# Performance work log

Measured on AMD Instinct MI355X. Metric: run time of the kernel, lower is better.

Reference implementation:

```python
import jax, jax.numpy as jnp
import numpy as np
import math

NUM_HEADS = 16
ROPE_BASE = 10000.0
SLIDING_WINDOW = 512  # note: original triu-then-tril composition makes the mask empty (no-op)


def _rope_cos_sin(seq_len, head_dim, dtype):
    inv_freq = 1.0 / (ROPE_BASE ** (jnp.arange(0, head_dim, 2, dtype=jnp.float32) / head_dim))
    t = jnp.arange(seq_len, dtype=jnp.float32)
    freqs = t[:, None] * inv_freq[None, :]          # [S, D/2]
    emb = jnp.concatenate([freqs, freqs], axis=-1)  # [S, D]
    # reshape to broadcast over [B, S, H, D]
    return jnp.cos(emb)[None, :, None, :].astype(dtype), jnp.sin(emb)[None, :, None, :].astype(dtype)


def _rotate_half(x):
    x1, x2 = jnp.split(x, 2, axis=-1)
    return jnp.concatenate([-x2, x1], axis=-1)


def setup_inputs() -> dict:
    key = jax.random.key(0)
    ks = jax.random.split(key, 9)
    B, S, E = 2, 2048, 2048
    sc = 1.0 / math.sqrt(E)
    return {
        "hidden_states": jax.random.normal(ks[0], (B, S, E), dtype=jnp.float32),
        "Wq": jax.random.normal(ks[1], (E, E), dtype=jnp.float32) * sc,
        "bq": jax.random.normal(ks[2], (E,), dtype=jnp.float32) * 0.01,
        "Wk": jax.random.normal(ks[3], (E, E), dtype=jnp.float32) * sc,
        "bk": jax.random.normal(ks[4], (E,), dtype=jnp.float32) * 0.01,
        "Wv": jax.random.normal(ks[5], (E, E), dtype=jnp.float32) * sc,
        "bv": jax.random.normal(ks[6], (E,), dtype=jnp.float32) * 0.01,
        "Wo": jax.random.normal(ks[7], (E, E), dtype=jnp.float32) * sc,
        "bo": jax.random.normal(ks[8], (E,), dtype=jnp.float32) * 0.01,
    }


def reference(hidden_states, Wq, bq, Wk, bk, Wv, bv, Wo, bo):
    B, S, E = hidden_states.shape
    H = NUM_HEADS
    D = E // H
    q = (hidden_states @ Wq.T + bq).reshape(B, S, H, D)
    k = (hidden_states @ Wk.T + bk).reshape(B, S, H, D)
    v = (hidden_states @ Wv.T + bv).reshape(B, S, H, D)

    cos, sin = _rope_cos_sin(S, D, q.dtype)
    q = q * cos + _rotate_half(q) * sin
    k = k * cos + _rotate_half(k) * sin

    scale = 1.0 / math.sqrt(D)
    scores = jnp.einsum("bqhd,bkhd->bhqk", q, k) * scale  # [B,H,S,S]
    # Faithful to source: triu(ones, +w) followed by tril(..., -w) is empty -> mask is a no-op.
    attn = jax.nn.softmax(scores, axis=-1)
    out = jnp.einsum("bhqk,bkhd->bqhd", attn, v).reshape(B, S, E)
    return out @ Wo.T + bo
```

## Files before the change

kernel.cpp:

```cpp
#include <hip/hip_runtime.h>
#include <hip/hip_bf16.h>

#define B_ 2
#define S_ 2048
#define E_ 2048
#define H_ 16
#define D_ 128
#define M_ (B_*S_)
#define NQKV_ (3*E_)

typedef __attribute__((ext_vector_type(8))) short bf16x8;
typedef __attribute__((ext_vector_type(4))) float f32x4;
typedef __attribute__((ext_vector_type(4))) unsigned short u16x4;
typedef __attribute__((ext_vector_type(2))) unsigned u32x2;

__device__ __forceinline__ unsigned short f2bf(float f) {
  union { float f; unsigned u; } v; v.f = f;
  unsigned r = v.u + 0x7fffu + ((v.u >> 16) & 1u);
  return (unsigned short)(r >> 16);
}
__device__ __forceinline__ float bf2f(unsigned short h) {
  union { unsigned u; float f; } v; v.u = ((unsigned)h) << 16;
  return v.f;
}

__device__ __forceinline__ void gload_lds16(const void* g, void* l) {
  __builtin_amdgcn_global_load_lds(
      (const __attribute__((address_space(1))) unsigned*)g,
      (__attribute__((address_space(3))) unsigned*)l, 16, 0, 0);
}

__global__ __launch_bounds__(256) void prep_kernel(
    const float* __restrict__ hs,
    const float* __restrict__ Wq, const float* __restrict__ Wk, const float* __restrict__ Wv,
    const float* __restrict__ Wo,
    const float* __restrict__ bq, const float* __restrict__ bk, const float* __restrict__ bv,
    unsigned short* __restrict__ hsb, unsigned short* __restrict__ Wqkv,
    unsigned short* __restrict__ Wob, float* __restrict__ biasqkv,
    float* __restrict__ cosT, float* __restrict__ sinT)
{
  const int seg = blockIdx.y;
  const int t0 = blockIdx.x * 256 + threadIdx.x;
  const int stride = gridDim.x * 256;
  if (seg == 0) {
    const int n = (M_*E_)/4;
    for (int i = t0; i < n; i += stride) {
      f32x4 v = ((const f32x4*)hs)[i];
      u16x4 o; o[0]=f2bf(v[0]); o[1]=f2bf(v[1]); o[2]=f2bf(v[2]); o[3]=f2bf(v[3]);
      ((u16x4*)hsb)[i] = o;
    }
  } else if (seg == 1) {
    const int n = (3*E_*E_)/4;
    for (int i = t0; i < n; i += stride) {
      int e4 = i << 2;
      int r = e4 >> 11;
      int k = e4 & 2047;
      const float* src = (r < E_) ? (Wq + ((size_t)r << 11) + k)
                       : (r < 2*E_) ? (Wk + ((size_t)(r - E_) << 11) + k)
                       : (Wv + ((size_t)(r - 2*E_) << 11) + k);
      f32x4 v = *(const f32x4*)src;
      u16x4 o; o[0]=f2bf(v[0]); o[1]=f2bf(v[1]); o[2]=f2bf(v[2]); o[3]=f2bf(v[3]);
      ((u16x4*)Wqkv)[i] = o;
    }
  } else if (seg == 2) {
    const int n = (E_*E_)/4;
    for (int i = t0; i < n; i += stride) {
      f32x4 v = ((const f32x4*)Wo)[i];
      u16x4 o; o[0]=f2bf(v[0]); o[1]=f2bf(v[1]); o[2]=f2bf(v[2]); o[3]=f2bf(v[3]);
      ((u16x4*)Wob)[i] = o;
    }
  } else if (seg == 3) {
    for (int i = t0; i < NQKV_; i += stride)
      biasqkv[i] = (i < E_) ? bq[i] : (i < 2*E_) ? bk[i - E_] : bv[i - 2*E_];
  } else {
    for (int i = t0; i < S_*64; i += stride) {
      int j = i & 63, s = i >> 6;
      float inv = exp2f(-(float)j * (13.287712379549449f / 64.0f));
      float ang = (float)s * inv;
      cosT[i] = cosf(ang);
      sinT[i] = sinf(ang);
    }
  }
}

#define STAGE8(basePtr, BUF, AB, KS, KT) do { \
    unsigned short* dst_ = lds + (BUF)*32768 + (AB)*16384 + (KS)*8192; \
    const unsigned short* src_ = (basePtr) + (KT)*64 + (KS)*32; \
    _Pragma("unroll") \
    for (int j_ = 0; j_ < 2; ++j_) { \
      int cc_ = (j_ << 9) + tid; \
      int row_ = cc_ >> 2, c2_ = cc_ & 3; \
      int sc_ = c2_ ^ ((row_ >> 1) & 3); \
      gload_lds16(src_ + (size_t)row_*K + sc_*8, (char*)dst_ + cc_*16); \
    } } while(0)

#define LOADA8(DST, MH, KS, BUF) do { \
    const unsigned short* Ab_ = lds + (BUF)*32768 + (KS)*8192; \
    _Pragma("unroll") \
    for (int j_ = 0; j_ < 4; ++j_) { \
      int row_ = wr*128 + ((MH)*4 + j_)*16 + l15; \
      DST[j_] = *(const bf16x8*)(Ab_ + row_*32 + ((l4 ^ ((row_>>1)&3)) << 3)); \
    } } while(0)

#define LOADB8(DST, KS, BUF) do { \
    const unsigned short* Bb_ = lds + (BUF)*32768 + 16384 + (KS)*8192; \
    _Pragma("unroll") \
    for (int j_ = 0; j_ < 4; ++j_) { \
      int row_ = wc*64 + j_*16 + l15; \
      DST[j_] = *(const bf16x8*)(Bb_ + row_*32 + ((l4 ^ ((row_>>1)&3)) << 3)); \
    } } while(0)

#define PRIO_MFMA(MH, AF, BF) do { \
    __builtin_amdgcn_s_setprio(1); \
    _Pragma("unroll") \
    for (int mm_ = 0; mm_ < 4; ++mm_) \
      _Pragma("unroll") \
      for (int nn_ = 0; nn_ < 4; ++nn_) \
        acc[(MH)*4+mm_][nn_] = __builtin_amdgcn_mfma_f32_16x16x32_bf16(AF[mm_], BF[nn_], acc[(MH)*4+mm_][nn_], 0,0,0); \
    __builtin_amdgcn_s_setprio(0); \
  } while(0)

#define BARPIN do { \
    __builtin_amdgcn_sched_barrier(0); \
    __builtin_amdgcn_s_barrier(); \
    __builtin_amdgcn_sched_barrier(0); \
  } while(0)

__global__ __launch_bounds__(512, 2) void gemm8(
    const unsigned short* __restrict__ A,
    const unsigned short* __restrict__ Bm,
    const float* __restrict__ bias,
    unsigned short* __restrict__ Cv,
    int M, int N, int K)
{
  __shared__ __align__(16) unsigned short lds[65536];
  const int tid = threadIdx.x;
  const int lane = tid & 63;
  const int w = tid >> 6;
  const int wr = w >> 2, wc = w & 3;
  const int l15 = lane & 15, l4 = lane >> 4;

  const int ntile = N >> 8;
  int wg = blockIdx.x;
  const int cpx = gridDim.x >> 3;
  wg = (wg & 7) * cpx + (wg >> 3);
  const int tm = wg / ntile, tn = wg % ntile;

  const unsigned short* Abase = A + ((size_t)tm*256)*K;
  const unsigned short* Bbase = Bm + ((size_t)tn*256)*K;

  f32x4 acc[8][4] = {};
  bf16x8 afA[4], afB[4], bfA[4], bfB[4];

  const int NITER = K >> 7;

  STAGE8(Bbase, 0, 1, 0, 0); STAGE8(Abase, 0, 0, 0, 0);
  STAGE8(Bbase, 0, 1, 1, 0); STAGE8(Abase, 0, 0, 1, 0);
  STAGE8(Bbase, 1, 1, 0, 1); STAGE8(Abase, 1, 0, 0, 1);
  STAGE8(Bbase, 1, 1, 1, 1);
  __builtin_amdgcn_sched_barrier(0);
  asm volatile("s_waitcnt vmcnt(6)" ::: "memory");
  __builtin_amdgcn_s_barrier();
  __builtin_amdgcn_sched_barrier(0);

  for (int i = 0; i < NITER; ++i) {
    const int t1k = 2*i + 1, t2k = 2*i + 2, t3k = 2*i + 3;
    const bool nl = (i < NITER - 1);
    STAGE8(Abase, 1, 0, 1, t1k);
    LOADA8(afA, 0, 0, 0); LOADB8(bfA, 0, 0);
    LOADA8(afB, 1, 0, 0);
    PRIO_MFMA(0, afA, bfA);
    BARPIN;
    if (nl) STAGE8(Bbase, 0, 1, 0, t2k);
    LOADA8(afA, 0, 1, 0); LOADB8(bfB, 1, 0);
    PRIO_MFMA(1, afB, bfA);
    BARPIN;
    if (nl) STAGE8(Abase, 0, 0, 0, t2k);
    LOADA8(afB, 1, 1, 0);
    PRIO_MFMA(0, afA, bfB);
    BARPIN;
    if (nl) STAGE8(Bbase, 0, 1, 1, t2k);
    PRIO_MFMA(1, afB, bfB);
    __builtin_amdgcn_sched_barrier(0);
    if (nl) asm volatile("s_waitcnt vmcnt(6)" ::: "memory");
    else    asm volatile("s_waitcnt vmcnt(0)" ::: "memory");
    __builtin_amdgcn_s_barrier();
    __builtin_amdgcn_sched_barrier(0);
    if (nl) STAGE8(Abase, 0, 0, 1, t2k);
    LOADA8(afA, 0, 0, 1); LOADB8(bfA, 0, 1);
    LOADA8(afB, 1, 0, 1);
    PRIO_MFMA(0, afA, bfA);
    BARPIN;
    if (nl) STAGE8(Bbase, 1, 1, 0, t3k);
    LOADA8(afA, 0, 1, 1); LOADB8(bfB, 1, 1);
    PRIO_MFMA(1, afB, bfA);
    BARPIN;
    if (nl) STAGE8(Abase, 1, 0, 0, t3k);
    LOADA8(afB, 1, 1, 1);
    PRIO_MFMA(0, afA, bfB);
    BARPIN;
    if (nl) STAGE8(Bbase, 1, 1, 1, t3k);
    PRIO_MFMA(1, afB, bfB);
    __builtin_amdgcn_sched_barrier(0);
    if (nl) asm volatile("s_waitcnt vmcnt(6)" ::: "memory");
    else    asm volatile("s_waitcnt vmcnt(0)" ::: "memory");
    __builtin_amdgcn_s_barrier();
    __builtin_amdgcn_sched_barrier(0);
  }

  #pragma unroll
  for (int mt = 0; mt < 8; ++mt) {
    #pragma unroll
    for (int nt = 0; nt < 4; ++nt) {
      int colg = tn*256 + wc*64 + nt*16 + l15;
      float bvv = bias[colg];
      #pragma unroll
      for (int r = 0; r < 4; ++r) {
        int rowg = tm*256 + wr*128 + mt*16 + l4*4 + r;
        Cv[(size_t)rowg*N + colg] = f2bf(acc[mt][nt][r] + bvv);
      }
    }
  }
}

template<int OUT_F32>
__global__ __launch_bounds__(256) void gemm_bt(
    const unsigned short* __restrict__ A,
    const unsigned short* __restrict__ Bm,
    const float* __restrict__ bias,
    void* __restrict__ Cv,
    int M, int N, int K)
{
  __shared__ unsigned short lA[128*64];
  __shared__ unsigned short lB[128*64];
  const int tid = threadIdx.x;
  const int lane = tid & 63;
  const int w = tid >> 6;
  const int wr = w >> 1, wc = w & 1;
  const int ntile = N >> 7;
  const int tm = blockIdx.x / ntile, tn = blockIdx.x % ntile;
  const int l15 = lane & 15, l4 = lane >> 4;

  f32x4 acc[4][4] = {};

  for (int kt = 0; kt < K; kt += 64) {
    #pragma unroll
    for (int i = 0; i < 4; ++i) {
      int cc = i*256 + tid;
      int row = cc >> 3, col = cc & 7;
      int scol = col ^ (row & 7);
      gload_lds16(A + (size_t)(tm*128 + row)*K + kt + scol*8, (char*)lA + cc*16);
    }
    #pragma unroll
    for (int i = 0; i < 4; ++i) {
      int cc = i*256 + tid;
      int row = cc >> 3, col = cc & 7;
      int scol = col ^ (row & 7);
      gload_lds16(Bm + (size_t)(tn*128 + row)*K + kt + scol*8, (char*)lB + cc*16);
    }
    asm volatile("s_waitcnt vmcnt(0)" ::: "memory");
    __syncthreads();

    #pragma unroll
    for (int ks = 0; ks < 2; ++ks) {
      bf16x8 af[4], bfr[4];
      #pragma unroll
      for (int mt = 0; mt < 4; ++mt) {
        int row = wr*64 + mt*16 + l15;
        int ch = (ks*4 + l4) ^ (row & 7);
        af[mt] = *(const bf16x8*)(lA + row*64 + ch*8);
      }
      #pragma unroll
      for (int nt = 0; nt < 4; ++nt) {
        int row = wc*64 + nt*16 + l15;
        int ch = (ks*4 + l4) ^ (row & 7);
        bfr[nt] = *(const bf16x8*)(lB + row*64 + ch*8);
      }
      #pragma unroll
      for (int mt = 0; mt < 4; ++mt)
        #pragma unroll
        for (int nt = 0; nt < 4; ++nt)
          acc[mt][nt] = __builtin_amdgcn_mfma_f32_16x16x32_bf16(af[mt], bfr[nt], acc[mt][nt], 0, 0, 0);
    }
    __syncthreads();
  }

  #pragma unroll
  for (int mt = 0; mt < 4; ++mt) {
    #pragma unroll
    for (int nt = 0; nt < 4; ++nt) {
      int colg = tn*128 + wc*64 + nt*16 + l15;
      float bvv = bias[colg];
      #pragma unroll
      for (int r = 0; r < 4; ++r) {
        int rowg = tm*128 + wr*64 + mt*16 + l4*4 + r;
        float v = acc[mt][nt][r] + bvv;
        if (OUT_F32) ((float*)Cv)[(size_t)rowg*N + colg] = v;
        else ((unsigned short*)Cv)[(size_t)rowg*N + colg] = f2bf(v);
      }
    }
  }
}

__global__ __launch_bounds__(256) void rope_kernel(
    unsigned short* __restrict__ qkv, const float* __restrict__ cosT, const float* __restrict__ sinT)
{
  int t = blockIdx.x*256 + threadIdx.x;
  int i  = t & 63;
  int h  = (t >> 6) & 15;
  int m  = t >> 10;
  int s  = m & (S_-1);
  float c = cosT[s*64 + i], sn = sinT[s*64 + i];
  const float scale = 0.08838834764831845f * 1.4426950408889634f;
  size_t base = (size_t)m*NQKV_ + h*128;
  float q1 = bf2f(qkv[base+i]), q2 = bf2f(qkv[base+64+i]);
  qkv[base+i]    = f2bf((q1*c - q2*sn)*scale);
  qkv[base+64+i] = f2bf((q2*c + q1*sn)*scale);
  size_t kb = base + E_;
  float k1 = bf2f(qkv[kb+i]), k2 = bf2f(qkv[kb+64+i]);
  qkv[kb+i]    = f2bf(k1*c - k2*sn);
  qkv[kb+64+i] = f2bf(k2*c + k1*sn);
}

__global__ __launch_bounds__(256) void transv_kernel(
    const unsigned short* __restrict__ qkv, unsigned short* __restrict__ Vt)
{
  __shared__ unsigned short t[32][33];
  int bid = blockIdx.x;
  int st = bid & 63;
  int dt = (bid >> 6) & 3;
  int bh = bid >> 8;
  int b = bh >> 4, h = bh & 15;
  int tx = threadIdx.x & 31, ty = threadIdx.x >> 5;
  #pragma unroll
  for (int j = 0; j < 4; ++j) {
    int r = ty + j*8;
    t[r][tx] = qkv[(size_t)(b*S_ + st*32 + r)*NQKV_ + 2*E_ + h*128 + dt*32 + tx];
  }
  __syncthreads();
  #pragma unroll
  for (int j = 0; j < 4; ++j) {
    int r = ty + j*8;
    Vt[((size_t)bh*D_ + dt*32 + r)*S_ + st*32 + tx] = t[tx][r];
  }
}

__global__ __launch_bounds__(256, 2) void attn_kernel(
    const unsigned short* __restrict__ qkv, const unsigned short* __restrict__ Vt,
    unsigned short* __restrict__ Ao)
{
  __shared__ unsigned short lK[64*128];
  __shared__ unsigned short lV[128*64];
  __shared__ __align__(16) unsigned short lP[4*32*64];
  int bid = blockIdx.x;
  bid = (bid & 7)*64 + (bid >> 3);
  const int qt = bid & 15;
  const int bh = bid >> 4;
  const int b = bh >> 4, h = bh & 15;
  const int tid = threadIdx.x, lane = tid & 63, w = tid >> 6;
  const int l15 = lane & 15, l4 = lane >> 4;

  bf16x8 qf[2][4];
  #pragma unroll
  for (int g = 0; g < 2; ++g) {
    const int qrow = qt*128 + w*32 + g*16 + l15;
    const unsigned short* qp = qkv + (size_t)(b*S_ + qrow)*NQKV_ + h*128 + l4*8;
    #pragma unroll
    for (int f = 0; f < 4; ++f) qf[g][f] = *(const bf16x8*)(qp + f*32);
  }

  f32x4 O[2][8];
  #pragma unroll
  for (int g = 0; g < 2; ++g)
    #pragma unroll
    for (int i = 0; i < 8; ++i) O[g][i] = (f32x4){0.f,0.f,0.f,0.f};
  float mx[2] = {-1e30f,-1e30f}, lsum[2] = {0.f,0.f};

  unsigned short* myP = lP + w*(32*64);
  const int ksw = (l15 & 7) << 3;
  const size_t kbase = (size_t)b*S_*NQKV_ + E_ + (size_t)h*128;
  const size_t vbase = (size_t)bh*D_*S_;

  for (int kt = 0; kt < S_; kt += 64) {
    #pragma unroll
    for (int i = 0; i < 4; ++i) {
      int cc = i*256 + tid;
      int row = cc >> 4, col = cc & 15;
      int scol = col ^ (row & 7);
      gload_lds16(qkv + kbase + (size_t)(kt + row)*NQKV_ + scol*8, (char*)lK + cc*16);
    }
    #pragma unroll
    for (int i = 0; i < 4; ++i) {
      int cc = i*256 + tid;
      int row = cc >> 3, col = cc & 7;
      int scol = col ^ ((row & 7) ^ ((row >> 3) & 7));
      gload_lds16(Vt + vbase + (size_t)row*S_ + kt + scol*8, (char*)lV + cc*16);
    }
    asm volatile("s_waitcnt vmcnt(0)" ::: "memory");
    __syncthreads();

    f32x4 sfr[2][4];
    #pragma unroll
    for (int nf = 0; nf < 4; ++nf) {
      f32x4 s0 = (f32x4){0.f,0.f,0.f,0.f};
      f32x4 s1 = (f32x4){0.f,0.f,0.f,0.f};
      #pragma unroll
      for (int ks = 0; ks < 4; ++ks) {
        int row = nf*16 + l15;
        int ch = (ks*4 + l4) ^ (row & 7);
        bf16x8 kf = *(const bf16x8*)(lK + row*128 + ch*8);
        s0 = __builtin_amdgcn_mfma_f32_16x16x32_bf16(kf, qf[0][ks], s0, 0, 0, 0);
        s1 = __builtin_amdgcn_mfma_f32_16x16x32_bf16(kf, qf[1][ks], s1, 0, 0, 0);
      }
      sfr[0][nf] = s0; sfr[1][nf] = s1;
    }

    float vm[2];
    #pragma unroll
    for (int g = 0; g < 2; ++g) {
      float v = -1e30f;
      #pragma unroll
      for (int nf = 0; nf < 4; ++nf)
        #pragma unroll
        for (int r = 0; r < 4; ++r) v = fmaxf(v, sfr[g][nf][r]);
      v = fmaxf(v, __shfl_xor(v, 16, 64));
      v = fmaxf(v, __shfl_xor(v, 32, 64));
      vm[g] = v;
    }

    if (__any((vm[0] > mx[0] + 8.0f) || (vm[1] > mx[1] + 8.0f))) {
      #pragma unroll
      for (int g = 0; g < 2; ++g) {
        float mn = fmaxf(mx[g], vm[g]);
        float al = __builtin_amdgcn_exp2f(mx[g] - mn);
        mx[g] = mn;
        lsum[g] *= al;
        #pragma unroll
        for (int r = 0; r < 4; ++r) {
          float ar = __shfl(al, (lane & 48) + l4*4 + r, 64);
          #pragma unroll
          for (int df = 0; df < 8; ++df) O[g][df][r] *= ar;
        }
      }
    }

    #pragma unroll
    for (int g = 0; g < 2; ++g) {
      float ps = 0.f;
      #pragma unroll
      for (int nf = 0; nf < 4; ++nf) {
        #pragma unroll
        for (int r = 0; r < 4; ++r) {
          float p = __builtin_amdgcn_exp2f(sfr[g][nf][r] - mx[g]);
          sfr[g][nf][r] = p;
          ps += p;
        }
      }
      ps += __shfl_xor(ps, 16, 64);
      ps += __shfl_xor(ps, 32, 64);
      lsum[g] += ps;
    }

    #pragma unroll
    for (int g = 0; g < 2; ++g) {
      #pragma unroll
      for (int nf = 0; nf < 4; ++nf) {
        unsigned lo = (unsigned)f2bf(sfr[g][nf][0]) | ((unsigned)f2bf(sfr[g][nf][1]) << 16);
        unsigned hi = (unsigned)f2bf(sfr[g][nf][2]) | ((unsigned)f2bf(sfr[g][nf][3]) << 16);
        int k0 = (nf*16 + l4*4) ^ ksw;
        u32x2 val; val[0] = lo; val[1] = hi;
        *(u32x2*)(myP + (g*16 + l15)*64 + k0) = val;
      }
    }
    asm volatile("s_waitcnt lgkmcnt(0)" ::: "memory");

    #pragma unroll
    for (int ks2 = 0; ks2 < 2; ++ks2) {
      int kk = (ks2*32 + l4*8) ^ ksw;
      bf16x8 pf0 = *(const bf16x8*)(myP + l15*64 + kk);
      bf16x8 pf1 = *(const bf16x8*)(myP + (16 + l15)*64 + kk);
      #pragma unroll
      for (int df = 0; df < 8; ++df) {
        int row = df*16 + l15;
        int ch = (ks2*4 + l4) ^ ((row & 7) ^ ((row >> 3) & 7));
        bf16x8 vf = *(const bf16x8*)(lV + row*64 + ch*8);
        O[0][df] = __builtin_amdgcn_mfma_f32_16x16x32_bf16(pf0, vf, O[0][df], 0, 0, 0);
        O[1][df] = __builtin_amdgcn_mfma_f32_16x16x32_bf16(pf1, vf, O[1][df], 0, 0, 0);
      }
    }
    __syncthreads();
  }

  #pragma unroll
  for (int g = 0; g < 2; ++g) {
    float linv = 1.0f / lsum[g];
    float inv[4];
    #pragma unroll
    for (int r = 0; r < 4; ++r) inv[r] = __shfl(linv, (lane & 48) + l4*4 + r, 64);
    #pragma unroll
    for (int df = 0; df < 8; ++df) {
      int colg = h*128 + df*16 + l15;
      #pragma unroll
      for (int r = 0; r < 4; ++r) {
        int rowg = qt*128 + w*32 + g*16 + l4*4 + r;
        Ao[(size_t)(b*S_ + rowg)*E_ + colg] = f2bf(O[g][df][r] * inv[r]);
      }
    }
  }
}

extern "C" void kernel_launch(void* const* d_in, const int* in_sizes, int n_in,
                              void* d_out, int out_size, void* d_ws, size_t ws_size,
                              hipStream_t stream) {
  const float* hs = (const float*)d_in[0];
  const float* Wq = (const float*)d_in[1];
  const float* bq = (const float*)d_in[2];
  const float* Wk = (const float*)d_in[3];
  const float* bk = (const float*)d_in[4];
  const float* Wv = (const float*)d_in[5];
  const float* bv = (const float*)d_in[6];
  const float* Wo = (const float*)d_in[7];
  const float* bo = (const float*)d_in[8];
  float* out = (float*)d_out;

  char* p = (char*)d_ws;
  auto alloc = [&](size_t bytes) { char* r = p; p += (bytes + 255) & ~(size_t)255; return r; };
  unsigned short* hsb  = (unsigned short*)alloc((size_t)M_*E_*2);
  unsigned short* Wqkv = (unsigned short*)alloc((size_t)NQKV_*E_*2);
  unsigned short* Wob  = (unsigned short*)alloc((size_t)E_*E_*2);
  unsigned short* qkv  = (unsigned short*)alloc((size_t)M_*NQKV_*2);
  unsigned short* Vt   = (unsigned short*)alloc((size_t)B_*H_*D_*S_*2);
  unsigned short* Ao   = (unsigned short*)alloc((size_t)M_*E_*2);
  float* biasqkv = (float*)alloc((size_t)NQKV_*4);
  float* cosT = (float*)alloc((size_t)S_*64*4);
  float* sinT = (float*)alloc((size_t)S_*64*4);

  prep_kernel<<<dim3(2048, 5), 256, 0, stream>>>(hs, Wq, Wk, Wv, Wo, bq, bk, bv,
      hsb, Wqkv, Wob, biasqkv, cosT, sinT);
  gemm8<<<dim3((M_/256)*(NQKV_/256)), 512, 0, stream>>>(hsb, Wqkv, biasqkv, qkv, M_, NQKV_, E_);
  rope_kernel<<<dim3((M_*H_*64)/256), 256, 0, stream>>>(qkv, cosT, sinT);
  transv_kernel<<<dim3(B_*H_*(D_/32)*(S_/32)), 256, 0, stream>>>(qkv, Vt);
  attn_kernel<<<dim3(B_*H_*(S_/128)), 256, 0, stream>>>(qkv, Vt, Ao);
  gemm_bt<1><<<dim3((M_/128)*(E_/128)), 256, 0, stream>>>(Ao, Wob, bo, out, M_, E_, E_);
}
```

Before: 296.0 us.

## Restructure GEMM main loop into eight barrier-separated load/MFMA phases

Replaces the GEMM inner loop's double-buffered register fragments (afA/afB, bfA/bfB) with a single af/bf set. Each of eight phases now issues its LDS fragment loads and the next global-to-LDS stage, then does a barrier and an lgkmcnt(0) wait, then runs a prioritized MFMA block and ends with a second barrier. The goal is a ping-pong schedule where waves on a SIMD alternate between memory and MFMA work, with lower register pressure. The cost is twice as many barriers per phase and no overlap of LDS reads with MFMA inside a single wave.

```diff
diff --git a/kernel.cpp b/kernel.cpp
--- a/kernel.cpp
+++ b/kernel.cpp
@@ -94,36 +94,46 @@
       gload_lds16(src_ + (size_t)row_*K + sc_*8, (char*)dst_ + cc_*16); \
     } } while(0)
 
-#define LOADA8(DST, MH, KS, BUF) do { \
+#define LOADA8(MH, KS, BUF) do { \
     const unsigned short* Ab_ = lds + (BUF)*32768 + (KS)*8192; \
     _Pragma("unroll") \
     for (int j_ = 0; j_ < 4; ++j_) { \
       int row_ = wr*128 + ((MH)*4 + j_)*16 + l15; \
-      DST[j_] = *(const bf16x8*)(Ab_ + row_*32 + ((l4 ^ ((row_>>1)&3)) << 3)); \
+      af[j_] = *(const bf16x8*)(Ab_ + row_*32 + ((l4 ^ ((row_>>1)&3)) << 3)); \
     } } while(0)
 
-#define LOADB8(DST, KS, BUF) do { \
+#define LOADB8(KS, BUF) do { \
     const unsigned short* Bb_ = lds + (BUF)*32768 + 16384 + (KS)*8192; \
     _Pragma("unroll") \
     for (int j_ = 0; j_ < 4; ++j_) { \
       int row_ = wc*64 + j_*16 + l15; \
-      DST[j_] = *(const bf16x8*)(Bb_ + row_*32 + ((l4 ^ ((row_>>1)&3)) << 3)); \
+      bf[j_] = *(const bf16x8*)(Bb_ + row_*32 + ((l4 ^ ((row_>>1)&3)) << 3)); \
     } } while(0)
 
-#define PRIO_MFMA(MH, AF, BF) do { \
-    __builtin_amdgcn_s_setprio(1); \
+#define MFMAQ(MH) do { \
     _Pragma("unroll") \
     for (int mm_ = 0; mm_ < 4; ++mm_) \
       _Pragma("unroll") \
       for (int nn_ = 0; nn_ < 4; ++nn_) \
-        acc[(MH)*4+mm_][nn_] = __builtin_amdgcn_mfma_f32_16x16x32_bf16(AF[mm_], BF[nn_], acc[(MH)*4+mm_][nn_], 0,0,0); \
-    __builtin_amdgcn_s_setprio(0); \
+        acc[(MH)*4+mm_][nn_] = __builtin_amdgcn_mfma_f32_16x16x32_bf16(af[mm_], bf[nn_], acc[(MH)*4+mm_][nn_], 0,0,0); \
   } while(0)
 
-#define BARPIN do { \
+#define WVM6 asm volatile("s_waitcnt vmcnt(6)" ::: "memory")
+#define WVM0 asm volatile("s_waitcnt vmcnt(0)" ::: "memory")
+
+#define PHASE(MH, KS, BUF, ISSUE, WAITV) do { \
+    LOADA8(MH, KS, BUF); \
+    if ((MH) == 0) LOADB8(KS, BUF); \
+    ISSUE; \
     __builtin_amdgcn_sched_barrier(0); \
     __builtin_amdgcn_s_barrier(); \
+    asm volatile("s_waitcnt lgkmcnt(0)" ::: "memory"); \
     __builtin_amdgcn_sched_barrier(0); \
+    __builtin_amdgcn_s_setprio(1); \
+    MFMAQ(MH); \
+    __builtin_amdgcn_s_setprio(0); \
+    WAITV; \
+    __builtin_amdgcn_s_barrier(); \
   } while(0)
 
 __global__ __launch_bounds__(512, 2) void gemm8(
@@ -150,7 +160,7 @@
   const unsigned short* Bbase = Bm + ((size_t)tn*256)*K;
 
   f32x4 acc[8][4] = {};
-  bf16x8 afA[4], afB[4], bfA[4], bfB[4];
+  bf16x8 af[4], bf[4];
 
   const int NITER = K >> 7;
 
@@ -159,53 +169,20 @@
   STAGE8(Bbase, 1, 1, 0, 1); STAGE8(Abase, 1, 0, 0, 1);
   STAGE8(Bbase, 1, 1, 1, 1);
   __builtin_amdgcn_sched_barrier(0);
-  asm volatile("s_waitcnt vmcnt(6)" ::: "memory");
+  WVM6;
   __builtin_amdgcn_s_barrier();
-  __builtin_amdgcn_sched_barrier(0);
 
   for (int i = 0; i < NITER; ++i) {
     const int t1k = 2*i + 1, t2k = 2*i + 2, t3k = 2*i + 3;
     const bool nl = (i < NITER - 1);
-    STAGE8(Abase, 1, 0, 1, t1k);
-    LOADA8(afA, 0, 0, 0); LOADB8(bfA, 0, 0);
-    LOADA8(afB, 1, 0, 0);
-    PRIO_MFMA(0, afA, bfA);
-    BARPIN;
-    if (nl) STAGE8(Bbase, 0, 1, 0, t2k);
-    LOADA8(afA, 0, 1, 0); LOADB8(bfB, 1, 0);
-    PRIO_MFMA(1, afB, bfA);
-    BARPIN;
-    if (nl) STAGE8(Abase, 0, 0, 0, t2k);
-    LOADA8(afB, 1, 1, 0);
-    PRIO_MFMA(0, afA, bfB);
-    BARPIN;
-    if (nl) STAGE8(Bbase, 0, 1, 1, t2k);
-    PRIO_MFMA(1, afB, bfB);
-    __builtin_amdgcn_sched_barrier(0);
-    if (nl) asm volatile("s_waitcnt vmcnt(6)" ::: "memory");
-    else    asm volatile("s_waitcnt vmcnt(0)" ::: "memory");
-    __builtin_amdgcn_s_barrier();
-    __builtin_amdgcn_sched_barrier(0);
-    if (nl) STAGE8(Abase, 0, 0, 1, t2k);
-    LOADA8(afA, 0, 0, 1); LOADB8(bfA, 0, 1);
-    LOADA8(afB, 1, 0, 1);
-    PRIO_MFMA(0, afA, bfA);
-    BARPIN;
-    if (nl) STAGE8(Bbase, 1, 1, 0, t3k);
-    LOADA8(afA, 0, 1, 1); LOADB8(bfB, 1, 1);
-    PRIO_MFMA(1, afB, bfA);
-    BARPIN;
-    if (nl) STAGE8(Abase, 1, 0, 0, t3k);
-    LOADA8(afB, 1, 1, 1);
-    PRIO_MFMA(0, afA, bfB);
-    BARPIN;
-    if (nl) STAGE8(Bbase, 1, 1, 1, t3k);
-    PRIO_MFMA(1, afB, bfB);
-    __builtin_amdgcn_sched_barrier(0);
-    if (nl) asm volatile("s_waitcnt vmcnt(6)" ::: "memory");
-    else    asm volatile("s_waitcnt vmcnt(0)" ::: "memory");
-    __builtin_amdgcn_s_barrier();
-    __builtin_amdgcn_sched_barrier(0);
+    PHASE(0, 0, 0, STAGE8(Abase, 1, 0, 1, t1k), );
+    PHASE(1, 0, 0, if (nl) STAGE8(Bbase, 0, 1, 0, t2k), );
+    PHASE(0, 1, 0, if (nl) STAGE8(Abase, 0, 0, 0, t2k), );
+    PHASE(1, 1, 0, if (nl) STAGE8(Bbase, 0, 1, 1, t2k), if (nl) WVM6; else WVM0);
+    PHASE(0, 0, 1, if (nl) STAGE8(Abase, 0, 0, 1, t2k), );
+    PHASE(1, 0, 1, if (nl) STAGE8(Bbase, 1, 1, 0, t3k), );
+    PHASE(0, 1, 1, if (nl) STAGE8(Abase, 1, 0, 0, t3k), );
+    PHASE(1, 1, 1, if (nl) STAGE8(Bbase, 1, 1, 1, t3k), if (nl) WVM6);
   }
 
   #pragma unroll
```

New measurement: 297.6 us. No clear change (+0.5%).
